# Kernel tuning notes

Measured on AMD Instinct MI355X. Metric: run time of the kernel, lower is better.

The kernel has to match this reference:

```python
import jax, jax.numpy as jnp
import numpy as np

D = 768
H = 12
EPS = 1e-5


def layer_norm(x, g, b):
    mu = jnp.mean(x, axis=-1, keepdims=True)
    var = jnp.var(x, axis=-1, keepdims=True)
    return (x - mu) * jax.lax.rsqrt(var + EPS) * g + b


def setup_inputs() -> dict:
    key = jax.random.key(0)
    ks = jax.random.split(key, 12)
    d, h = D, H
    x = jax.random.normal(ks[0], (4, 1024, d), dtype=jnp.float32)
    # attention projections (per-head dim is full d, per the module)
    s_qkv = (6.0 / (d + d * h)) ** 0.5  # xavier-like scale
    Wq = jax.random.uniform(ks[1], (d, d * h), jnp.float32, -s_qkv, s_qkv)
    Wk = jax.random.uniform(ks[2], (d, d * h), jnp.float32, -s_qkv, s_qkv)
    Wv = jax.random.uniform(ks[3], (d, d * h), jnp.float32, -s_qkv, s_qkv)
    Wu = jax.random.uniform(ks[4], (d * h, d), jnp.float32, -s_qkv, s_qkv)
    bu = jnp.zeros((d,), jnp.float32)
    # MLP
    s1 = (6.0 / (d + 4 * d)) ** 0.5
    W1 = jax.random.uniform(ks[5], (d, 4 * d), jnp.float32, -s1, s1)
    b1 = jax.random.normal(ks[6], (4 * d,), jnp.float32) * 1e-6
    W2 = jax.random.uniform(ks[7], (4 * d, d), jnp.float32, -s1, s1)
    b2 = jax.random.normal(ks[8], (d,), jnp.float32) * 1e-6
    ln1_g = jnp.ones((d,), jnp.float32)
    ln1_b = jnp.zeros((d,), jnp.float32)
    ln2_g = jnp.ones((d,), jnp.float32)
    ln2_b = jnp.zeros((d,), jnp.float32)
    return dict(x=x, Wq=Wq, Wk=Wk, Wv=Wv, Wu=Wu, bu=bu,
                ln1_g=ln1_g, ln1_b=ln1_b, ln2_g=ln2_g, ln2_b=ln2_b,
                W1=W1, b1=b1, W2=W2, b2=b2)


def reference(x, Wq, Wk, Wv, Wu, bu, ln1_g, ln1_b, ln2_g, ln2_b, W1, b1, W2, b2):
    b, n, d = x.shape
    h = H
    # --- pre-LN attention block ---
    res = x
    y = layer_norm(x, ln1_g, ln1_b)
    qs = (y @ Wq).reshape(b, n, h, d)  # per-head dim = d (module quirk)
    ks = (y @ Wk).reshape(b, n, h, d)
    vs = (y @ Wv).reshape(b, n, h, d)
    scores = jnp.einsum('bihd,bjhd->bhij', qs, ks) / (d ** 0.5)
    w = jax.nn.softmax(scores, axis=-1)
    att = jnp.einsum('bhij,bjhd->bihd', w, vs).reshape(b, n, h * d)
    y = att @ Wu + bu
    x = y + res
    # --- pre-LN MLP block (dropout is identity at inference) ---
    res = x
    y = layer_norm(x, ln2_g, ln2_b)
    y = jax.nn.relu(y @ W1 + b1)
    y = y @ W2 + b2
    return y + res
```

## Files before the change

### kernel.cpp

```cpp
#include <hip/hip_runtime.h>
#include <cstdint>
#include <cmath>


typedef __bf16 bf16_t;
typedef __bf16 bf16x8 __attribute__((ext_vector_type(8)));
typedef __bf16 bf16x4 __attribute__((ext_vector_type(4)));
typedef float floatx4 __attribute__((ext_vector_type(4)));

#define DMODEL 768
#define NHEAD  12
#define SEQ    1024
#define NBATCH 4
#define ROWS   (NBATCH*SEQ)
#define DH     (DMODEL*NHEAD)
#define DFF    (4*DMODEL)

template<bool BIAS, bool RES, bool RELU, int OMODE>
__global__ __launch_bounds__(256)
void gemm_v6(const bf16_t* __restrict__ A, const bf16_t* __restrict__ BT,
             void* __restrict__ Cv, int K, int lda, int ldb, int ldc,
             int bdiv, long sa_hi, long sa_lo, long sb_hi, long sb_lo,
             long sc_hi, long sc_lo,
             const float* __restrict__ bias, const float* __restrict__ res,
             int ldres, float alpha)
{
  __shared__ __align__(16) bf16_t As[128*64];
  __shared__ __align__(16) bf16_t Bs[128*64];

  const int tid  = threadIdx.x;
  const int wave = tid >> 6;
  const int lane = tid & 63;
  const int r    = lane & 15;
  const int q    = lane >> 4;

  const int z = blockIdx.z;
  A  += (long)(z / bdiv) * sa_hi + (long)(z % bdiv) * sa_lo;
  BT += (long)(z / bdiv) * sb_hi + (long)(z % bdiv) * sb_lo;
  const long coff = (long)(z / bdiv) * sc_hi + (long)(z % bdiv) * sc_lo;

  const int bm = blockIdx.y * 128;
  const int bn = blockIdx.x * 128;
  const int wm = (wave & 1) * 64;
  const int wn = (wave >> 1) * 64;

  const int blk0 = 2*wave, blk1 = 2*wave + 1;
  const bf16_t* a_src0 = A  + (long)(bm + blk0*16 + r) * lda + q*8;
  const bf16_t* a_src1 = A  + (long)(bm + blk1*16 + r) * lda + q*8;
  const bf16_t* b_src0 = BT + (long)(bn + blk0*16 + r) * ldb + q*8;
  const bf16_t* b_src1 = BT + (long)(bn + blk1*16 + r) * ldb + q*8;
  const int da0 = blk0*512 + lane*8;
  const int da1 = blk1*512 + lane*8;

  const int am = (wave & 1) * 4;
  const int bb = (wave >> 1) * 4;

  floatx4 acc[4][4] = {};

  for (int k0 = 0; k0 < K; k0 += 64) {
    bf16x8 a00 = *(const bf16x8*)(a_src0 + k0);
    bf16x8 a01 = *(const bf16x8*)(a_src0 + k0 + 32);
    bf16x8 a10 = *(const bf16x8*)(a_src1 + k0);
    bf16x8 a11 = *(const bf16x8*)(a_src1 + k0 + 32);
    bf16x8 b00 = *(const bf16x8*)(b_src0 + k0);
    bf16x8 b01 = *(const bf16x8*)(b_src0 + k0 + 32);
    bf16x8 b10 = *(const bf16x8*)(b_src1 + k0);
    bf16x8 b11 = *(const bf16x8*)(b_src1 + k0 + 32);
    *(bf16x8*)(As + da0)        = a00;
    *(bf16x8*)(As + 4096 + da0) = a01;
    *(bf16x8*)(As + da1)        = a10;
    *(bf16x8*)(As + 4096 + da1) = a11;
    *(bf16x8*)(Bs + da0)        = b00;
    *(bf16x8*)(Bs + 4096 + da0) = b01;
    *(bf16x8*)(Bs + da1)        = b10;
    *(bf16x8*)(Bs + 4096 + da1) = b11;
    __syncthreads();
#pragma unroll
    for (int p = 0; p < 2; ++p) {
      bf16x8 afrag[4], bfrag[4];
#pragma unroll
      for (int t = 0; t < 4; ++t) {
        afrag[t] = *(const bf16x8*)(As + p*4096 + (am + t)*512 + lane*8);
        bfrag[t] = *(const bf16x8*)(Bs + p*4096 + (bb + t)*512 + lane*8);
      }
#pragma unroll
      for (int mt = 0; mt < 4; ++mt)
#pragma unroll
        for (int nt = 0; nt < 4; ++nt)
          acc[mt][nt] = __builtin_amdgcn_mfma_f32_16x16x32_bf16(
              afrag[mt], bfrag[nt], acc[mt][nt], 0, 0, 0);
    }
    __syncthreads();
  }

  const int row0 = bm + wm + q*4;
  const int col0 = bn + wn + r;
#pragma unroll
  for (int nt = 0; nt < 4; ++nt) {
    const int col = col0 + nt*16;
    float bv = 0.f;
    if (BIAS) bv = bias[col];
#pragma unroll
    for (int mt = 0; mt < 4; ++mt) {
#pragma unroll
      for (int e = 0; e < 4; ++e) {
        const int rowi = row0 + mt*16 + e;
        float v = acc[mt][nt][e] * alpha;
        if (BIAS) v += bv;
        if (RELU) v = fmaxf(v, 0.f);
        if (RES)  v += res[(long)rowi * ldres + col];
        const long idx = coff + (long)rowi * ldc + col;
        if (OMODE == 0)      ((bf16_t*)Cv)[idx] = (bf16_t)v;
        else if (OMODE == 1) ((float*)Cv)[idx] = v;
        else                 ((float*)Cv)[idx] += v;
      }
    }
  }
}

__global__ void tr_f2b_v6(const float* __restrict__ in, bf16_t* __restrict__ out,
                          int ldi, int ldo)
{
  __shared__ bf16_t tile[32][34];
  const int c0 = blockIdx.x * 32, r0 = blockIdx.y * 32;
  const int tx = threadIdx.x, ty = threadIdx.y;
#pragma unroll
  for (int i = 0; i < 4; ++i)
    tile[ty + 8*i][tx] = (bf16_t)in[(long)(r0 + ty + 8*i) * ldi + c0 + tx];
  __syncthreads();
#pragma unroll
  for (int i = 0; i < 4; ++i)
    out[(long)(c0 + ty + 8*i) * ldo + r0 + tx] = tile[tx][ty + 8*i];
}

__global__ void tr_b_v6(const bf16_t* __restrict__ in, bf16_t* __restrict__ out,
                        int ldi, int ldo, int bdiv,
                        long si_hi, long si_lo, long so_hi, long so_lo)
{
  __shared__ bf16_t tile[32][34];
  const int z = blockIdx.z;
  in  += (long)(z / bdiv) * si_hi + (long)(z % bdiv) * si_lo;
  out += (long)(z / bdiv) * so_hi + (long)(z % bdiv) * so_lo;
  const int c0 = blockIdx.x * 32, r0 = blockIdx.y * 32;
  const int tx = threadIdx.x, ty = threadIdx.y;
#pragma unroll
  for (int i = 0; i < 4; ++i)
    tile[ty + 8*i][tx] = in[(long)(r0 + ty + 8*i) * ldi + c0 + tx];
  __syncthreads();
#pragma unroll
  for (int i = 0; i < 4; ++i)
    out[(long)(c0 + ty + 8*i) * ldo + r0 + tx] = tile[tx][ty + 8*i];
}

__global__ void tr_wh_v6(const float* __restrict__ Wq, const float* __restrict__ Wk,
                         const float* __restrict__ Wv, const float* __restrict__ Wu,
                         bf16_t* __restrict__ WhT, bf16_t* __restrict__ WuTh, int h)
{
  __shared__ bf16_t tile[32][34];
  const int z = blockIdx.z;
  const float* in; bf16_t* out; int ldi;
  if (z < 3) {
    const float* W = (z == 0) ? Wq : (z == 1) ? Wk : Wv;
    in  = W + (long)h * DMODEL;
    ldi = DH;
    out = WhT + (long)z * DMODEL * DMODEL;
  } else {
    in  = Wu + (long)h * DMODEL * DMODEL;
    ldi = DMODEL;
    out = WuTh;
  }
  const int c0 = blockIdx.x * 32, r0 = blockIdx.y * 32;
  const int tx = threadIdx.x, ty = threadIdx.y;
#pragma unroll
  for (int i = 0; i < 4; ++i)
    tile[ty + 8*i][tx] = (bf16_t)in[(long)(r0 + ty + 8*i) * ldi + c0 + tx];
  __syncthreads();
#pragma unroll
  for (int i = 0; i < 4; ++i)
    out[(long)(c0 + ty + 8*i) * DMODEL + r0 + tx] = tile[tx][ty + 8*i];
}

__global__ void cast3_v6(const float* __restrict__ a, const float* __restrict__ b,
                         const float* __restrict__ c,
                         bf16_t* __restrict__ oa, bf16_t* __restrict__ ob,
                         bf16_t* __restrict__ oc)
{
  const float* src = (blockIdx.z == 0) ? a : (blockIdx.z == 1) ? b : c;
  bf16_t* dst      = (blockIdx.z == 0) ? oa : (blockIdx.z == 1) ? ob : oc;
  const long i = ((long)blockIdx.x * 256 + threadIdx.x) * 4;
  float4 v = *(const float4*)(src + i);
  bf16x4 o;
  o[0] = (bf16_t)v.x; o[1] = (bf16_t)v.y; o[2] = (bf16_t)v.z; o[3] = (bf16_t)v.w;
  *(bf16x4*)(dst + i) = o;
}

__global__ void cast1_v6(const float* __restrict__ src, bf16_t* __restrict__ dst)
{
  const long i = ((long)blockIdx.x * 256 + threadIdx.x) * 4;
  float4 v = *(const float4*)(src + i);
  bf16x4 o;
  o[0] = (bf16_t)v.x; o[1] = (bf16_t)v.y; o[2] = (bf16_t)v.z; o[3] = (bf16_t)v.w;
  *(bf16x4*)(dst + i) = o;
}

__global__ void ln_v6(const float* __restrict__ x, const float* __restrict__ g,
                      const float* __restrict__ b, bf16_t* __restrict__ y)
{
  const long row = blockIdx.x;
  const int tid = threadIdx.x;
  const float* xr = x + row * DMODEL;
  float v0 = xr[tid], v1 = xr[tid + 256], v2 = xr[tid + 512];
  float s  = v0 + v1 + v2;
  float ss = v0*v0 + v1*v1 + v2*v2;
  for (int o = 32; o; o >>= 1) { s += __shfl_down(s, o); ss += __shfl_down(ss, o); }
  __shared__ float rs[4], rss[4];
  const int wave = tid >> 6, lane = tid & 63;
  if (lane == 0) { rs[wave] = s; rss[wave] = ss; }
  __syncthreads();
  s  = rs[0] + rs[1] + rs[2] + rs[3];
  ss = rss[0] + rss[1] + rss[2] + rss[3];
  const float inv = 1.0f / (float)DMODEL;
  const float mean = s * inv;
  const float var  = ss * inv - mean * mean;
  const float rstd = rsqrtf(var + 1e-5f);
  bf16_t* yr = y + row * DMODEL;
  yr[tid]       = (bf16_t)(((v0 - mean) * rstd) * g[tid]       + b[tid]);
  yr[tid + 256] = (bf16_t)(((v1 - mean) * rstd) * g[tid + 256] + b[tid + 256]);
  yr[tid + 512] = (bf16_t)(((v2 - mean) * rstd) * g[tid + 512] + b[tid + 512]);
}

__global__ void softmax_v6(bf16_t* __restrict__ S)
{
  const long row = blockIdx.x;
  const int tid = threadIdx.x;
  bf16_t* p = S + row * SEQ + tid * 4;
  bf16x4 v = *(const bf16x4*)p;
  float f0 = (float)v[0], f1 = (float)v[1], f2 = (float)v[2], f3 = (float)v[3];
  float m = fmaxf(fmaxf(f0, f1), fmaxf(f2, f3));
  for (int o = 32; o; o >>= 1) m = fmaxf(m, __shfl_down(m, o));
  __shared__ float rm[4], rsum[4];
  const int wave = tid >> 6, lane = tid & 63;
  if (lane == 0) rm[wave] = m;
  __syncthreads();
  m = fmaxf(fmaxf(rm[0], rm[1]), fmaxf(rm[2], rm[3]));
  float e0 = __expf(f0 - m), e1 = __expf(f1 - m), e2 = __expf(f2 - m), e3 = __expf(f3 - m);
  float s = e0 + e1 + e2 + e3;
  for (int o = 32; o; o >>= 1) s += __shfl_down(s, o);
  if (lane == 0) rsum[wave] = s;
  __syncthreads();
  s = rsum[0] + rsum[1] + rsum[2] + rsum[3];
  const float invs = 1.0f / s;
  bf16x4 o4;
  o4[0] = (bf16_t)(e0 * invs); o4[1] = (bf16_t)(e1 * invs);
  o4[2] = (bf16_t)(e2 * invs); o4[3] = (bf16_t)(e3 * invs);
  *(bf16x4*)p = o4;
}

__global__ void finalize_v6(const float* __restrict__ acc, const float* __restrict__ add,
                            const float* __restrict__ bias, float* __restrict__ o)
{
  const long i = (long)blockIdx.x * 256 + threadIdx.x;
  const int c = (int)(i % DMODEL);
  o[i] = acc[i] + bias[c] + add[i];
}

template<int NP>
__global__ void reduce_v6(const float* __restrict__ p, const float* __restrict__ add,
                          const float* __restrict__ bias, float* __restrict__ o,
                          long plane)
{
  const long i = ((long)blockIdx.x * 256 + threadIdx.x) * 4;
  float4 s = *(const float4*)(p + i);
#pragma unroll
  for (int n = 1; n < NP; ++n) {
    float4 v = *(const float4*)(p + i + (long)n * plane);
    s.x += v.x; s.y += v.y; s.z += v.z; s.w += v.w;
  }
  const int c = (int)(i % DMODEL);
  float4 bv = *(const float4*)(bias + c);
  float4 av = *(const float4*)(add + i);
  float4 r;
  r.x = s.x + bv.x + av.x; r.y = s.y + bv.y + av.y;
  r.z = s.z + bv.z + av.z; r.w = s.w + bv.w + av.w;
  *(float4*)(o + i) = r;
}

extern "C" void kernel_launch(void* const* d_in, const int* in_sizes, int n_in,
                              void* d_out, int out_size, void* d_ws, size_t ws_size,
                              hipStream_t stream)
{
  (void)in_sizes; (void)n_in; (void)out_size;
  const float* x    = (const float*)d_in[0];
  const float* Wq   = (const float*)d_in[1];
  const float* Wk   = (const float*)d_in[2];
  const float* Wv   = (const float*)d_in[3];
  const float* Wu   = (const float*)d_in[4];
  const float* bu   = (const float*)d_in[5];
  const float* ln1g = (const float*)d_in[6];
  const float* ln1b = (const float*)d_in[7];
  const float* ln2g = (const float*)d_in[8];
  const float* ln2b = (const float*)d_in[9];
  const float* W1   = (const float*)d_in[10];
  const float* b1   = (const float*)d_in[11];
  const float* W2   = (const float*)d_in[12];
  const float* b2   = (const float*)d_in[13];
  float* out = (float*)d_out;

  char* ws = (char*)d_ws;
  size_t off = 0;
  auto alloc = [&](size_t bytes) -> void* {
    void* p = (void*)(ws + off);
    off += (bytes + 255) & ~(size_t)255;
    return p;
  };

  const float qk_alpha = 1.0f / sqrtf((float)DMODEL);
  dim3 tb(32, 8);

  const size_t SZ_W   = (size_t)DMODEL * DH * 2;
  const size_t SZ_MT  = (size_t)NHEAD * DMODEL * DMODEL * 2;
  const size_t SZ_Y   = (size_t)ROWS * DMODEL * 2;
  const size_t SZ_X2  = (size_t)ROWS * DMODEL * 4;

  if (ws_size >= (size_t)299e6) {
    bf16_t* MT   = (bf16_t*)alloc(SZ_MT);
    bf16_t* PhT  = (bf16_t*)alloc(SZ_MT);
    bf16_t* y    = (bf16_t*)alloc(SZ_Y);
    float*  x2f  = (float* )alloc(SZ_X2);
    bf16_t* T    = (bf16_t*)alloc((size_t)NBATCH * NHEAD * SEQ * DMODEL * 2);
    bf16_t* S    = (bf16_t*)alloc((size_t)NBATCH * SEQ * NHEAD * SEQ * 2);
    bf16_t* Zt   = (bf16_t*)alloc((size_t)NBATCH * DMODEL * NHEAD * SEQ * 2);
    bf16_t* Wqb  = (bf16_t*)T;
    bf16_t* Wkb  = (bf16_t*)((char*)T + SZ_W);
    bf16_t* Wvb  = (bf16_t*)((char*)T + 2*SZ_W);
    bf16_t* WuT  = (bf16_t*)((char*)T + 3*SZ_W);
    float*  part = (float*)T;
    bf16_t* W1T  = (bf16_t*)S;
    bf16_t* W2T  = (bf16_t*)((char*)S + 4718592);
    bf16_t* t    = (bf16_t*)((char*)S + 9437184);
    float*  partM= (float* )((char*)S + 34603008);
    bf16_t* y2   = (bf16_t*)Zt;

    cast3_v6<<<dim3(6912, 1, 3), 256, 0, stream>>>(Wq, Wk, Wv, Wqb, Wkb, Wvb);
    tr_f2b_v6<<<dim3(DMODEL/32, DH/32), tb, 0, stream>>>(Wu, WuT, DMODEL, DH);
    gemm_v6<false,false,false,0><<<dim3(6, 6, NHEAD), 256, 0, stream>>>(
        Wkb, Wqb, MT, DMODEL, DH, DH, DMODEL, NHEAD,
        0, DMODEL, 0, DMODEL, 0, (long)DMODEL*DMODEL, nullptr, nullptr, 0, 1.0f);
    gemm_v6<false,false,false,0><<<dim3(6, 6, NHEAD), 256, 0, stream>>>(
        WuT, Wvb, PhT, DMODEL, DH, DH, DMODEL, NHEAD,
        0, DMODEL, 0, DMODEL, 0, (long)DMODEL*DMODEL, nullptr, nullptr, 0, 1.0f);

    ln_v6<<<ROWS, 256, 0, stream>>>(x, ln1g, ln1b, y);
    gemm_v6<false,false,false,0><<<dim3(6, 8, NBATCH*NHEAD), 256, 0, stream>>>(
        y, MT, T, DMODEL, DMODEL, DMODEL, DMODEL, NHEAD,
        (long)SEQ*DMODEL, 0, 0, (long)DMODEL*DMODEL,
        (long)NHEAD*SEQ*DMODEL, (long)SEQ*DMODEL, nullptr, nullptr, 0, 1.0f);
    gemm_v6<false,false,false,0><<<dim3(8, 8, NBATCH*NHEAD), 256, 0, stream>>>(
        T, y, S, DMODEL, DMODEL, DMODEL, NHEAD*SEQ, NHEAD,
        (long)NHEAD*SEQ*DMODEL, (long)SEQ*DMODEL, (long)SEQ*DMODEL, 0,
        (long)SEQ*NHEAD*SEQ, (long)SEQ, nullptr, nullptr, 0, qk_alpha);
    softmax_v6<<<NBATCH*SEQ*NHEAD, 256, 0, stream>>>(S);
    gemm_v6<false,false,false,0><<<dim3(8, 6, NBATCH*NHEAD), 256, 0, stream>>>(
        PhT, y, Zt, DMODEL, DMODEL, DMODEL, NHEAD*SEQ, NHEAD,
        0, (long)DMODEL*DMODEL, (long)SEQ*DMODEL, 0,
        (long)DMODEL*NHEAD*SEQ, (long)SEQ, nullptr, nullptr, 0, 1.0f);
    gemm_v6<false,false,false,1><<<dim3(6, 8, 24), 256, 0, stream>>>(
        S, Zt, part, NHEAD*SEQ/6, NHEAD*SEQ, NHEAD*SEQ, DMODEL, NBATCH,
        (long)(NHEAD*SEQ/6), (long)SEQ*NHEAD*SEQ,
        (long)(NHEAD*SEQ/6), (long)DMODEL*NHEAD*SEQ,
        (long)ROWS*DMODEL, (long)SEQ*DMODEL, nullptr, nullptr, 0, 1.0f);
    reduce_v6<6><<<(ROWS*DMODEL)/1024, 256, 0, stream>>>(
        part, x, bu, x2f, (long)ROWS*DMODEL);

    tr_f2b_v6<<<dim3(DFF/32, DMODEL/32), tb, 0, stream>>>(W1, W1T, DFF, DMODEL);
    tr_f2b_v6<<<dim3(DMODEL/32, DFF/32), tb, 0, stream>>>(W2, W2T, DMODEL, DFF);
    ln_v6<<<ROWS, 256, 0, stream>>>(x2f, ln2g, ln2b, y2);
    gemm_v6<true,false,true,0><<<dim3(DFF/128, ROWS/128, 1), 256, 0, stream>>>(
        y2, W1T, t, DMODEL, DMODEL, DMODEL, DFF, 1, 0,0,0,0,0,0, b1, nullptr, 0, 1.0f);
    gemm_v6<false,false,false,1><<<dim3(6, ROWS/128, 2), 256, 0, stream>>>(
        t, W2T, partM, DFF/2, DFF, DFF, DMODEL, 2,
        0, (long)(DFF/2), 0, (long)(DFF/2), 0, (long)ROWS*DMODEL,
        nullptr, nullptr, 0, 1.0f);
    reduce_v6<2><<<(ROWS*DMODEL)/1024, 256, 0, stream>>>(
        partM, x2f, b2, out, (long)ROWS*DMODEL);
  } else if (ws_size >= (size_t)112e6) {
    bf16_t* MT  = (bf16_t*)alloc(SZ_MT);
    bf16_t* PhT = (bf16_t*)alloc(SZ_MT);
    bf16_t* y   = (bf16_t*)alloc(SZ_Y);
    float*  x2f = (float* )alloc(SZ_X2);
    char*   BIG = (char*  )alloc((size_t)62914560);
    bf16_t* T_b  = (bf16_t*)(BIG);
    bf16_t* S_b  = (bf16_t*)(BIG + 18874368);
    bf16_t* Zt_b = (bf16_t*)(BIG + 44040192);
    float*  part = (float* )(BIG);
    bf16_t* Wqb = (bf16_t*)(BIG);
    bf16_t* Wkb = (bf16_t*)(BIG + SZ_W);
    bf16_t* Wvb = (bf16_t*)(BIG + 2*SZ_W);
    bf16_t* WuT = (bf16_t*)(BIG + 3*SZ_W);
    bf16_t* W1T   = (bf16_t*)(BIG);
    bf16_t* W2T   = (bf16_t*)(BIG + 4718592);
    bf16_t* t     = (bf16_t*)(BIG + 9437184);
    float*  partM = (float* )(BIG + 34603008);
    bf16_t* y2    = y;

    cast3_v6<<<dim3(6912, 1, 3), 256, 0, stream>>>(Wq, Wk, Wv, Wqb, Wkb, Wvb);
    tr_f2b_v6<<<dim3(DMODEL/32, DH/32), tb, 0, stream>>>(Wu, WuT, DMODEL, DH);
    gemm_v6<false,false,false,0><<<dim3(6, 6, NHEAD), 256, 0, stream>>>(
        Wkb, Wqb, MT, DMODEL, DH, DH, DMODEL, NHEAD,
        0, DMODEL, 0, DMODEL, 0, (long)DMODEL*DMODEL, nullptr, nullptr, 0, 1.0f);
    gemm_v6<false,false,false,0><<<dim3(6, 6, NHEAD), 256, 0, stream>>>(
        WuT, Wvb, PhT, DMODEL, DH, DH, DMODEL, NHEAD,
        0, DMODEL, 0, DMODEL, 0, (long)DMODEL*DMODEL, nullptr, nullptr, 0, 1.0f);

    ln_v6<<<ROWS, 256, 0, stream>>>(x, ln1g, ln1b, y);
    for (int b = 0; b < NBATCH; ++b) {
      const bf16_t* yb = y + (long)b * SEQ * DMODEL;
      gemm_v6<false,false,false,0><<<dim3(6, 8, NHEAD), 256, 0, stream>>>(
          yb, MT, T_b, DMODEL, DMODEL, DMODEL, DMODEL, NHEAD,
          0, 0, 0, (long)DMODEL*DMODEL, 0, (long)SEQ*DMODEL,
          nullptr, nullptr, 0, 1.0f);
      gemm_v6<false,false,false,0><<<dim3(8, 8, NHEAD), 256, 0, stream>>>(
          T_b, yb, S_b, DMODEL, DMODEL, DMODEL, NHEAD*SEQ, NHEAD,
          0, (long)SEQ*DMODEL, 0, 0, 0, (long)SEQ,
          nullptr, nullptr, 0, qk_alpha);
      softmax_v6<<<NHEAD*SEQ, 256, 0, stream>>>(S_b);
      gemm_v6<false,false,false,0><<<dim3(8, 6, NHEAD), 256, 0, stream>>>(
          PhT, yb, Zt_b, DMODEL, DMODEL, DMODEL, NHEAD*SEQ, NHEAD,
          0, (long)DMODEL*DMODEL, 0, 0, 0, (long)SEQ,
          nullptr, nullptr, 0, 1.0f);
      gemm_v6<false,false,false,1><<<dim3(6, 8, 6), 256, 0, stream>>>(
          S_b, Zt_b, part, NHEAD*SEQ/6, NHEAD*SEQ, NHEAD*SEQ, DMODEL, 6,
          0, (long)(NHEAD*SEQ/6), 0, (long)(NHEAD*SEQ/6), 0, (long)SEQ*DMODEL,
          nullptr, nullptr, 0, 1.0f);
      reduce_v6<6><<<(SEQ*DMODEL)/1024, 256, 0, stream>>>(
          part, x + (long)b*SEQ*DMODEL, bu, x2f + (long)b*SEQ*DMODEL,
          (long)SEQ*DMODEL);
    }

    tr_f2b_v6<<<dim3(DFF/32, DMODEL/32), tb, 0, stream>>>(W1, W1T, DFF, DMODEL);
    tr_f2b_v6<<<dim3(DMODEL/32, DFF/32), tb, 0, stream>>>(W2, W2T, DMODEL, DFF);
    ln_v6<<<ROWS, 256, 0, stream>>>(x2f, ln2g, ln2b, y2);
    gemm_v6<true,false,true,0><<<dim3(DFF/128, ROWS/128, 1), 256, 0, stream>>>(
        y2, W1T, t, DMODEL, DMODEL, DMODEL, DFF, 1, 0,0,0,0,0,0, b1, nullptr, 0, 1.0f);
    gemm_v6<false,false,false,1><<<dim3(6, ROWS/128, 2), 256, 0, stream>>>(
        t, W2T, partM, DFF/2, DFF, DFF, DMODEL, 2,
        0, (long)(DFF/2), 0, (long)(DFF/2), 0, (long)ROWS*DMODEL,
        nullptr, nullptr, 0, 1.0f);
    reduce_v6<2><<<(ROWS*DMODEL)/1024, 256, 0, stream>>>(
        partM, x2f, b2, out, (long)ROWS*DMODEL);
  } else if (ws_size >= (size_t)70e6) {
    bf16_t* MT  = (bf16_t*)alloc(SZ_MT);
    bf16_t* PhT = (bf16_t*)alloc(SZ_MT);
    bf16_t* y   = (bf16_t*)alloc(SZ_Y);
    char*   R   = (char*  )alloc((size_t)33554432);
    bf16_t* WAb = (bf16_t*)(R);
    bf16_t* WBb = (bf16_t*)(R + SZ_W);
    float*  x2f = (float* )(R);
    bf16_t* T_h = (bf16_t*)(R + 12582912);
    bf16_t* S_h = (bf16_t*)(R + 18874368);
    bf16_t* Z_h = (bf16_t*)(R + 27262976);
    bf16_t* W1T = (bf16_t*)(R + 12582912);
    bf16_t* W2T = (bf16_t*)(R + 17301504);
    bf16_t* t   = (bf16_t*)MT;
    bf16_t* y2  = y;

    cast1_v6<<<6912, 256, 0, stream>>>(Wq, WAb);
    cast1_v6<<<6912, 256, 0, stream>>>(Wk, WBb);
    gemm_v6<false,false,false,0><<<dim3(6, 6, NHEAD), 256, 0, stream>>>(
        WBb, WAb, MT, DMODEL, DH, DH, DMODEL, NHEAD,
        0, DMODEL, 0, DMODEL, 0, (long)DMODEL*DMODEL, nullptr, nullptr, 0, 1.0f);
    cast1_v6<<<6912, 256, 0, stream>>>(Wv, WAb);
    tr_f2b_v6<<<dim3(DMODEL/32, DH/32), tb, 0, stream>>>(Wu, WBb, DMODEL, DH);
    gemm_v6<false,false,false,0><<<dim3(6, 6, NHEAD), 256, 0, stream>>>(
        WBb, WAb, PhT, DMODEL, DH, DH, DMODEL, NHEAD,
        0, DMODEL, 0, DMODEL, 0, (long)DMODEL*DMODEL, nullptr, nullptr, 0, 1.0f);

    ln_v6<<<ROWS, 256, 0, stream>>>(x, ln1g, ln1b, y);
    for (int h = 0; h < NHEAD; ++h) {
      const bf16_t* MTh  = MT  + (long)h * DMODEL * DMODEL;
      const bf16_t* PhTh = PhT + (long)h * DMODEL * DMODEL;
      gemm_v6<false,false,false,0><<<dim3(6, ROWS/128, 1), 256, 0, stream>>>(
          y, MTh, T_h, DMODEL, DMODEL, DMODEL, DMODEL, 1,
          0,0,0,0,0,0, nullptr, nullptr, 0, 1.0f);
      gemm_v6<false,false,false,0><<<dim3(8, 8, NBATCH), 256, 0, stream>>>(
          T_h, y, S_h, DMODEL, DMODEL, DMODEL, SEQ, NBATCH,
          0, (long)SEQ*DMODEL, 0, (long)SEQ*DMODEL, 0, (long)SEQ*SEQ,
          nullptr, nullptr, 0, qk_alpha);
      softmax_v6<<<ROWS, 256, 0, stream>>>(S_h);
      gemm_v6<false,false,false,0><<<dim3(8, 6, NBATCH), 256, 0, stream>>>(
          PhTh, y, Z_h, DMODEL, DMODEL, DMODEL, SEQ, NBATCH,
          0, 0, 0, (long)SEQ*DMODEL, 0, (long)DMODEL*SEQ,
          nullptr, nullptr, 0, 1.0f);
      if (h == 0)
        gemm_v6<false,false,false,1><<<dim3(6, 8, NBATCH), 256, 0, stream>>>(
            S_h, Z_h, x2f, SEQ, SEQ, SEQ, DMODEL, NBATCH,
            0, (long)SEQ*SEQ, 0, (long)DMODEL*SEQ, 0, (long)SEQ*DMODEL,
            nullptr, nullptr, 0, 1.0f);
      else
        gemm_v6<false,false,false,2><<<dim3(6, 8, NBATCH), 256, 0, stream>>>(
            S_h, Z_h, x2f, SEQ, SEQ, SEQ, DMODEL, NBATCH,
            0, (long)SEQ*SEQ, 0, (long)DMODEL*SEQ, 0, (long)SEQ*DMODEL,
            nullptr, nullptr, 0, 1.0f);
    }
    finalize_v6<<<(ROWS*DMODEL)/256, 256, 0, stream>>>(x2f, x, bu, x2f);

    tr_f2b_v6<<<dim3(DFF/32, DMODEL/32), tb, 0, stream>>>(W1, W1T, DFF, DMODEL);
    tr_f2b_v6<<<dim3(DMODEL/32, DFF/32), tb, 0, stream>>>(W2, W2T, DMODEL, DFF);
    ln_v6<<<ROWS, 256, 0, stream>>>(x2f, ln2g, ln2b, y2);
    gemm_v6<true,false,true,0><<<dim3(DFF/128, ROWS/128, 1), 256, 0, stream>>>(
        y2, W1T, t, DMODEL, DMODEL, DMODEL, DFF, 1, 0,0,0,0,0,0, b1, nullptr, 0, 1.0f);
    gemm_v6<true,true,false,1><<<dim3(6, ROWS/128, 1), 256, 0, stream>>>(
        t, W2T, out, DFF/2, DFF, DFF, DMODEL, 1, 0,0,0,0,0,0,
        b2, x2f, DMODEL, 1.0f);
    gemm_v6<false,false,false,2><<<dim3(6, ROWS/128, 1), 256, 0, stream>>>(
        t + DFF/2, W2T + DFF/2, out, DFF/2, DFF, DFF, DMODEL, 1, 0,0,0,0,0,0,
        nullptr, nullptr, 0, 1.0f);
  } else {
    bf16_t* W1T   = (bf16_t*)alloc((size_t)DMODEL * DFF * 2);
    bf16_t* W2T   = (bf16_t*)alloc((size_t)DMODEL * DFF * 2);
    bf16_t* y     = (bf16_t*)alloc(SZ_Y);
    float*  x2f   = (float* )alloc(SZ_X2);
    char*   reg1  = (char*)alloc((size_t)3*DMODEL*DMODEL*2 + (size_t)DMODEL*DMODEL*2 + (size_t)SEQ*DMODEL*2);
    bf16_t* WhT   = (bf16_t*)reg1;
    bf16_t* WuTh  = (bf16_t*)(reg1 + (size_t)3*DMODEL*DMODEL*2);
    bf16_t* attb  = (bf16_t*)(reg1 + (size_t)4*DMODEL*DMODEL*2);
    bf16_t* y2    = (bf16_t*)reg1;
    char*   reg2  = (char*)alloc((size_t)SEQ*3*DMODEL*2 + (size_t)DMODEL*SEQ*2 + (size_t)SEQ*SEQ*2);
    bf16_t* QKVb  = (bf16_t*)reg2;
    bf16_t* Vtb   = (bf16_t*)(reg2 + (size_t)SEQ*3*DMODEL*2);
    bf16_t* Sb    = (bf16_t*)(reg2 + (size_t)SEQ*3*DMODEL*2 + (size_t)DMODEL*SEQ*2);
    bf16_t* tslab = (bf16_t*)reg2;

    tr_f2b_v6<<<dim3(DFF/32, DMODEL/32), tb, 0, stream>>>(W1, W1T, DFF, DMODEL);
    tr_f2b_v6<<<dim3(DMODEL/32, DFF/32), tb, 0, stream>>>(W2, W2T, DMODEL, DFF);
    ln_v6<<<ROWS, 256, 0, stream>>>(x, ln1g, ln1b, y);

    const int N3 = 3 * DMODEL;
    for (int h = 0; h < NHEAD; ++h) {
      tr_wh_v6<<<dim3(24, 24, 4), tb, 0, stream>>>(Wq, Wk, Wv, Wu, WhT, WuTh, h);
      for (int b = 0; b < NBATCH; ++b) {
        const bf16_t* yb = y + (size_t)b * SEQ * DMODEL;
        gemm_v6<false,false,false,0><<<dim3(N3/128, SEQ/128, 1), 256, 0, stream>>>(
            yb, WhT, QKVb, DMODEL, DMODEL, DMODEL, N3, 1, 0,0,0,0,0,0,
            nullptr, nullptr, 0, 1.0f);
        tr_b_v6<<<dim3(DMODEL/32, SEQ/32, 1), tb, 0, stream>>>(
            QKVb + 2*DMODEL, Vtb, N3, SEQ, 1, 0,0,0,0);
        gemm_v6<false,false,false,0><<<dim3(SEQ/128, SEQ/128, 1), 256, 0, stream>>>(
            QKVb, QKVb + DMODEL, Sb, DMODEL, N3, N3, SEQ, 1, 0,0,0,0,0,0,
            nullptr, nullptr, 0, qk_alpha);
        softmax_v6<<<SEQ, 256, 0, stream>>>(Sb);
        gemm_v6<false,false,false,0><<<dim3(DMODEL/128, SEQ/128, 1), 256, 0, stream>>>(
            Sb, Vtb, attb, SEQ, SEQ, SEQ, DMODEL, 1, 0,0,0,0,0,0,
            nullptr, nullptr, 0, 1.0f);
        float* x2b = x2f + (size_t)b * SEQ * DMODEL;
        if (h == 0)
          gemm_v6<false,false,false,1><<<dim3(DMODEL/128, SEQ/128, 1), 256, 0, stream>>>(
              attb, WuTh, x2b, DMODEL, DMODEL, DMODEL, DMODEL, 1, 0,0,0,0,0,0,
              nullptr, nullptr, 0, 1.0f);
        else
          gemm_v6<false,false,false,2><<<dim3(DMODEL/128, SEQ/128, 1), 256, 0, stream>>>(
              attb, WuTh, x2b, DMODEL, DMODEL, DMODEL, DMODEL, 1, 0,0,0,0,0,0,
              nullptr, nullptr, 0, 1.0f);
      }
    }
    finalize_v6<<<(ROWS*DMODEL)/256, 256, 0, stream>>>(x2f, x, bu, x2f);
    ln_v6<<<ROWS, 256, 0, stream>>>(x2f, ln2g, ln2b, y2);
    for (int kb = 0; kb < 4; ++kb) {
      gemm_v6<true,false,true,0><<<dim3(DMODEL/128, ROWS/128, 1), 256, 0, stream>>>(
          y2, W1T + (size_t)kb*DMODEL*DMODEL, tslab, DMODEL, DMODEL, DMODEL, DMODEL, 1,
          0,0,0,0,0,0, b1 + kb*DMODEL, nullptr, 0, 1.0f);
      if (kb == 0)
        gemm_v6<true,true,false,1><<<dim3(DMODEL/128, ROWS/128, 1), 256, 0, stream>>>(
            tslab, W2T + (size_t)kb*DMODEL, out, DMODEL, DMODEL, DFF, DMODEL, 1,
            0,0,0,0,0,0, b2, x2f, DMODEL, 1.0f);
      else
        gemm_v6<false,false,false,2><<<dim3(DMODEL/128, ROWS/128, 1), 256, 0, stream>>>(
            tslab, W2T + (size_t)kb*DMODEL, out, DMODEL, DMODEL, DFF, DMODEL, 1,
            0,0,0,0,0,0, nullptr, nullptr, 0, 1.0f);
    }
  }
}
```

Before: 1.170 ms.

## Shrink top-tier workspace by batching T per batch and reducing split-K partials

In the largest-workspace path, the per-head T intermediate is no longer stored for all batches. T is now computed per batch into a reused buffer, and the weight copies are aliased into the S region, which lowers the threshold for that path from 299e6 to 262e6 bytes. The S·Zt split-K drops from 6 to 3 partials, which halves the partial buffer and the reduce traffic but gives fewer blocks. The W2 split-K rises from 2 to 4 partials for more parallelism, at the cost of more partial writes. All kernels are renamed from v6 to v7. Which branch runs depends on the workspace size the harness provides.

Result: faster. 1.047 ms (-10.5%).

```diff
diff --git a/kernel.cpp b/kernel.cpp
--- a/kernel.cpp
+++ b/kernel.cpp
@@ -18,7 +18,7 @@
 
 template<bool BIAS, bool RES, bool RELU, int OMODE>
 __global__ __launch_bounds__(256)
-void gemm_v6(const bf16_t* __restrict__ A, const bf16_t* __restrict__ BT,
+void gemm_v7(const bf16_t* __restrict__ A, const bf16_t* __restrict__ BT,
              void* __restrict__ Cv, int K, int lda, int ldb, int ldc,
              int bdiv, long sa_hi, long sa_lo, long sb_hi, long sb_lo,
              long sc_hi, long sc_lo,
@@ -118,7 +118,7 @@
   }
 }
 
-__global__ void tr_f2b_v6(const float* __restrict__ in, bf16_t* __restrict__ out,
+__global__ void tr_f2b_v7(const float* __restrict__ in, bf16_t* __restrict__ out,
                           int ldi, int ldo)
 {
   __shared__ bf16_t tile[32][34];
@@ -133,7 +133,7 @@
     out[(long)(c0 + ty + 8*i) * ldo + r0 + tx] = tile[tx][ty + 8*i];
 }
 
-__global__ void tr_b_v6(const bf16_t* __restrict__ in, bf16_t* __restrict__ out,
+__global__ void tr_b_v7(const bf16_t* __restrict__ in, bf16_t* __restrict__ out,
                         int ldi, int ldo, int bdiv,
                         long si_hi, long si_lo, long so_hi, long so_lo)
 {
@@ -152,7 +152,7 @@
     out[(long)(c0 + ty + 8*i) * ldo + r0 + tx] = tile[tx][ty + 8*i];
 }
 
-__global__ void tr_wh_v6(const float* __restrict__ Wq, const float* __restrict__ Wk,
+__global__ void tr_wh_v7(const float* __restrict__ Wq, const float* __restrict__ Wk,
                          const float* __restrict__ Wv, const float* __restrict__ Wu,
                          bf16_t* __restrict__ WhT, bf16_t* __restrict__ WuTh, int h)
 {
@@ -180,7 +180,7 @@
     out[(long)(c0 + ty + 8*i) * DMODEL + r0 + tx] = tile[tx][ty + 8*i];
 }
 
-__global__ void cast3_v6(const float* __restrict__ a, const float* __restrict__ b,
+__global__ void cast3_v7(const float* __restrict__ a, const float* __restrict__ b,
                          const float* __restrict__ c,
                          bf16_t* __restrict__ oa, bf16_t* __restrict__ ob,
                          bf16_t* __restrict__ oc)
@@ -194,7 +194,7 @@
   *(bf16x4*)(dst + i) = o;
 }
 
-__global__ void cast1_v6(const float* __restrict__ src, bf16_t* __restrict__ dst)
+__global__ void cast1_v7(const float* __restrict__ src, bf16_t* __restrict__ dst)
 {
   const long i = ((long)blockIdx.x * 256 + threadIdx.x) * 4;
   float4 v = *(const float4*)(src + i);
@@ -203,7 +203,7 @@
   *(bf16x4*)(dst + i) = o;
 }
 
-__global__ void ln_v6(const float* __restrict__ x, const float* __restrict__ g,
+__global__ void ln_v7(const float* __restrict__ x, const float* __restrict__ g,
                       const float* __restrict__ b, bf16_t* __restrict__ y)
 {
   const long row = blockIdx.x;
@@ -229,7 +229,7 @@
   yr[tid + 512] = (bf16_t)(((v2 - mean) * rstd) * g[tid + 512] + b[tid + 512]);
 }
 
-__global__ void softmax_v6(bf16_t* __restrict__ S)
+__global__ void softmax_v7(bf16_t* __restrict__ S)
 {
   const long row = blockIdx.x;
   const int tid = threadIdx.x;
@@ -256,7 +256,7 @@
   *(bf16x4*)p = o4;
 }
 
-__global__ void finalize_v6(const float* __restrict__ acc, const float* __restrict__ add,
+__global__ void finalize_v7(const float* __restrict__ acc, const float* __restrict__ add,
                             const float* __restrict__ bias, float* __restrict__ o)
 {
   const long i = (long)blockIdx.x * 256 + threadIdx.x;
@@ -265,7 +265,7 @@
 }
 
 template<int NP>
-__global__ void reduce_v6(const float* __restrict__ p, const float* __restrict__ add,
+__global__ void reduce_v7(const float* __restrict__ p, const float* __restrict__ add,
                           const float* __restrict__ bias, float* __restrict__ o,
                           long plane)
 {
@@ -322,66 +322,69 @@
   const size_t SZ_Y   = (size_t)ROWS * DMODEL * 2;
   const size_t SZ_X2  = (size_t)ROWS * DMODEL * 4;
 
-  if (ws_size >= (size_t)299e6) {
+  if (ws_size >= (size_t)262e6) {
     bf16_t* MT   = (bf16_t*)alloc(SZ_MT);
     bf16_t* PhT  = (bf16_t*)alloc(SZ_MT);
     bf16_t* y    = (bf16_t*)alloc(SZ_Y);
     float*  x2f  = (float* )alloc(SZ_X2);
-    bf16_t* T    = (bf16_t*)alloc((size_t)NBATCH * NHEAD * SEQ * DMODEL * 2);
+    float*  part = (float* )alloc((size_t)3 * ROWS * DMODEL * 4);
     bf16_t* S    = (bf16_t*)alloc((size_t)NBATCH * SEQ * NHEAD * SEQ * 2);
     bf16_t* Zt   = (bf16_t*)alloc((size_t)NBATCH * DMODEL * NHEAD * SEQ * 2);
-    bf16_t* Wqb  = (bf16_t*)T;
-    bf16_t* Wkb  = (bf16_t*)((char*)T + SZ_W);
-    bf16_t* Wvb  = (bf16_t*)((char*)T + 2*SZ_W);
-    bf16_t* WuT  = (bf16_t*)((char*)T + 3*SZ_W);
-    float*  part = (float*)T;
+    bf16_t* T_b  = (bf16_t*)part;
+    bf16_t* Wqb  = (bf16_t*)S;
+    bf16_t* Wkb  = (bf16_t*)((char*)S + SZ_W);
+    bf16_t* Wvb  = (bf16_t*)((char*)S + 2*SZ_W);
+    bf16_t* WuT  = (bf16_t*)((char*)S + 3*SZ_W);
     bf16_t* W1T  = (bf16_t*)S;
     bf16_t* W2T  = (bf16_t*)((char*)S + 4718592);
     bf16_t* t    = (bf16_t*)((char*)S + 9437184);
     float*  partM= (float* )((char*)S + 34603008);
     bf16_t* y2   = (bf16_t*)Zt;
 
-    cast3_v6<<<dim3(6912, 1, 3), 256, 0, stream>>>(Wq, Wk, Wv, Wqb, Wkb, Wvb);
-    tr_f2b_v6<<<dim3(DMODEL/32, DH/32), tb, 0, stream>>>(Wu, WuT, DMODEL, DH);
-    gemm_v6<false,false,false,0><<<dim3(6, 6, NHEAD), 256, 0, stream>>>(
+    cast3_v7<<<dim3(6912, 1, 3), 256, 0, stream>>>(Wq, Wk, Wv, Wqb, Wkb, Wvb);
+    tr_f2b_v7<<<dim3(DMODEL/32, DH/32), tb, 0, stream>>>(Wu, WuT, DMODEL, DH);
+    gemm_v7<false,false,false,0><<<dim3(6, 6, NHEAD), 256, 0, stream>>>(
         Wkb, Wqb, MT, DMODEL, DH, DH, DMODEL, NHEAD,
         0, DMODEL, 0, DMODEL, 0, (long)DMODEL*DMODEL, nullptr, nullptr, 0, 1.0f);
-    gemm_v6<false,false,false,0><<<dim3(6, 6, NHEAD), 256, 0, stream>>>(
+    gemm_v7<false,false,false,0><<<dim3(6, 6, NHEAD), 256, 0, stream>>>(
         WuT, Wvb, PhT, DMODEL, DH, DH, DMODEL, NHEAD,
         0, DMODEL, 0, DMODEL, 0, (long)DMODEL*DMODEL, nullptr, nullptr, 0, 1.0f);
 
-    ln_v6<<<ROWS, 256, 0, stream>>>(x, ln1g, ln1b, y);
-    gemm_v6<false,false,false,0><<<dim3(6, 8, NBATCH*NHEAD), 256, 0, stream>>>(
-        y, MT, T, DMODEL, DMODEL, DMODEL, DMODEL, NHEAD,
-        (long)SEQ*DMODEL, 0, 0, (long)DMODEL*DMODEL,
-        (long)NHEAD*SEQ*DMODEL, (long)SEQ*DMODEL, nullptr, nullptr, 0, 1.0f);
-    gemm_v6<false,false,false,0><<<dim3(8, 8, NBATCH*NHEAD), 256, 0, stream>>>(
-        T, y, S, DMODEL, DMODEL, DMODEL, NHEAD*SEQ, NHEAD,
-        (long)NHEAD*SEQ*DMODEL, (long)SEQ*DMODEL, (long)SEQ*DMODEL, 0,
-        (long)SEQ*NHEAD*SEQ, (long)SEQ, nullptr, nullptr, 0, qk_alpha);
-    softmax_v6<<<NBATCH*SEQ*NHEAD, 256, 0, stream>>>(S);
-    gemm_v6<false,false,false,0><<<dim3(8, 6, NBATCH*NHEAD), 256, 0, stream>>>(
+    ln_v7<<<ROWS, 256, 0, stream>>>(x, ln1g, ln1b, y);
+    for (int b = 0; b < NBATCH; ++b) {
+      const bf16_t* yb = y + (long)b * SEQ * DMODEL;
+      gemm_v7<false,false,false,0><<<dim3(6, 8, NHEAD), 256, 0, stream>>>(
+          yb, MT, T_b, DMODEL, DMODEL, DMODEL, DMODEL, NHEAD,
+          0, 0, 0, (long)DMODEL*DMODEL, 0, (long)SEQ*DMODEL,
+          nullptr, nullptr, 0, 1.0f);
+      gemm_v7<false,false,false,0><<<dim3(8, 8, NHEAD), 256, 0, stream>>>(
+          T_b, yb, S + (long)b*SEQ*NHEAD*SEQ, DMODEL, DMODEL, DMODEL, NHEAD*SEQ, NHEAD,
+          0, (long)SEQ*DMODEL, 0, 0, 0, (long)SEQ,
+          nullptr, nullptr, 0, qk_alpha);
+    }
+    softmax_v7<<<NBATCH*SEQ*NHEAD, 256, 0, stream>>>(S);
+    gemm_v7<false,false,false,0><<<dim3(8, 6, NBATCH*NHEAD), 256, 0, stream>>>(
         PhT, y, Zt, DMODEL, DMODEL, DMODEL, NHEAD*SEQ, NHEAD,
         0, (long)DMODEL*DMODEL, (long)SEQ*DMODEL, 0,
         (long)DMODEL*NHEAD*SEQ, (long)SEQ, nullptr, nullptr, 0, 1.0f);
-    gemm_v6<false,false,false,1><<<dim3(6, 8, 24), 256, 0, stream>>>(
-        S, Zt, part, NHEAD*SEQ/6, NHEAD*SEQ, NHEAD*SEQ, DMODEL, NBATCH,
-        (long)(NHEAD*SEQ/6), (long)SEQ*NHEAD*SEQ,
-        (long)(NHEAD*SEQ/6), (long)DMODEL*NHEAD*SEQ,
+    gemm_v7<false,false,false,1><<<dim3(6, 8, 12), 256, 0, stream>>>(
+        S, Zt, part, NHEAD*SEQ/3, NHEAD*SEQ, NHEAD*SEQ, DMODEL, NBATCH,
+        (long)(NHEAD*SEQ/3), (long)SEQ*NHEAD*SEQ,
+        (long)(NHEAD*SEQ/3), (long)DMODEL*NHEAD*SEQ,
         (long)ROWS*DMODEL, (long)SEQ*DMODEL, nullptr, nullptr, 0, 1.0f);
-    reduce_v6<6><<<(ROWS*DMODEL)/1024, 256, 0, stream>>>(
+    reduce_v7<3><<<(ROWS*DMODEL)/1024, 256, 0, stream>>>(
         part, x, bu, x2f, (long)ROWS*DMODEL);
 
-    tr_f2b_v6<<<dim3(DFF/32, DMODEL/32), tb, 0, stream>>>(W1, W1T, DFF, DMODEL);
-    tr_f2b_v6<<<dim3(DMODEL/32, DFF/32), tb, 0, stream>>>(W2, W2T, DMODEL, DFF);
-    ln_v6<<<ROWS, 256, 0, stream>>>(x2f, ln2g, ln2b, y2);
-    gemm_v6<true,false,true,0><<<dim3(DFF/128, ROWS/128, 1), 256, 0, stream>>>(
+    tr_f2b_v7<<<dim3(DFF/32, DMODEL/32), tb, 0, stream>>>(W1, W1T, DFF, DMODEL);
+    tr_f2b_v7<<<dim3(DMODEL/32, DFF/32), tb, 0, stream>>>(W2, W2T, DMODEL, DFF);
+    ln_v7<<<ROWS, 256, 0, stream>>>(x2f, ln2g, ln2b, y2);
+    gemm_v7<true,false,true,0><<<dim3(DFF/128, ROWS/128, 1), 256, 0, stream>>>(
         y2, W1T, t, DMODEL, DMODEL, DMODEL, DFF, 1, 0,0,0,0,0,0, b1, nullptr, 0, 1.0f);
-    gemm_v6<false,false,false,1><<<dim3(6, ROWS/128, 2), 256, 0, stream>>>(
-        t, W2T, partM, DFF/2, DFF, DFF, DMODEL, 2,
-        0, (long)(DFF/2), 0, (long)(DFF/2), 0, (long)ROWS*DMODEL,
+    gemm_v7<false,false,false,1><<<dim3(6, ROWS/128, 4), 256, 0, stream>>>(
+        t, W2T, partM, DFF/4, DFF, DFF, DMODEL, 4,
+        0, (long)(DFF/4), 0, (long)(DFF/4), 0, (long)ROWS*DMODEL,
         nullptr, nullptr, 0, 1.0f);
-    reduce_v6<2><<<(ROWS*DMODEL)/1024, 256, 0, stream>>>(
+    reduce_v7<4><<<(ROWS*DMODEL)/1024, 256, 0, stream>>>(
         partM, x2f, b2, out, (long)ROWS*DMODEL);
   } else if (ws_size >= (size_t)112e6) {
     bf16_t* MT  = (bf16_t*)alloc(SZ_MT);
@@ -403,50 +406,50 @@
     float*  partM = (float* )(BIG + 34603008);
     bf16_t* y2    = y;
 
-    cast3_v6<<<dim3(6912, 1, 3), 256, 0, stream>>>(Wq, Wk, Wv, Wqb, Wkb, Wvb);
-    tr_f2b_v6<<<dim3(DMODEL/32, DH/32), tb, 0, stream>>>(Wu, WuT, DMODEL, DH);
-    gemm_v6<false,false,false,0><<<dim3(6, 6, NHEAD), 256, 0, stream>>>(
+    cast3_v7<<<dim3(6912, 1, 3), 256, 0, stream>>>(Wq, Wk, Wv, Wqb, Wkb, Wvb);
+    tr_f2b_v7<<<dim3(DMODEL/32, DH/32), tb, 0, stream>>>(Wu, WuT, DMODEL, DH);
+    gemm_v7<false,false,false,0><<<dim3(6, 6, NHEAD), 256, 0, stream>>>(
         Wkb, Wqb, MT, DMODEL, DH, DH, DMODEL, NHEAD,
         0, DMODEL, 0, DMODEL, 0, (long)DMODEL*DMODEL, nullptr, nullptr, 0, 1.0f);
-    gemm_v6<false,false,false,0><<<dim3(6, 6, NHEAD), 256, 0, stream>>>(
+    gemm_v7<false,false,false,0><<<dim3(6, 6, NHEAD), 256, 0, stream>>>(
         WuT, Wvb, PhT, DMODEL, DH, DH, DMODEL, NHEAD,
         0, DMODEL, 0, DMODEL, 0, (long)DMODEL*DMODEL, nullptr, nullptr, 0, 1.0f);
 
-    ln_v6<<<ROWS, 256, 0, stream>>>(x, ln1g, ln1b, y);
+    ln_v7<<<ROWS, 256, 0, stream>>>(x, ln1g, ln1b, y);
     for (int b = 0; b < NBATCH; ++b) {
       const bf16_t* yb = y + (long)b * SEQ * DMODEL;
-      gemm_v6<false,false,false,0><<<dim3(6, 8, NHEAD), 256, 0, stream>>>(
+      gemm_v7<false,false,false,0><<<dim3(6, 8, NHEAD), 256, 0, stream>>>(
           yb, MT, T_b, DMODEL, DMODEL, DMODEL, DMODEL, NHEAD,
           0, 0, 0, (long)DMODEL*DMODEL, 0, (long)SEQ*DMODEL,
           nullptr, nullptr, 0, 1.0f);
-      gemm_v6<false,false,false,0><<<dim3(8, 8, NHEAD), 256, 0, stream>>>(
+      gemm_v7<false,false,false,0><<<dim3(8, 8, NHEAD), 256, 0, stream>>>(
           T_b, yb, S_b, DMODEL, DMODEL, DMODEL, NHEAD*SEQ, NHEAD,
           0, (long)SEQ*DMODEL, 0, 0, 0, (long)SEQ,
           nullptr, nullptr, 0, qk_alpha);
-      softmax_v6<<<NHEAD*SEQ, 256, 0, stream>>>(S_b);
-      gemm_v6<false,false,false,0><<<dim3(8, 6, NHEAD), 256, 0, stream>>>(
+      softmax_v7<<<NHEAD*SEQ, 256, 0, stream>>>(S_b);
+      gemm_v7<false,false,false,0><<<dim3(8, 6, NHEAD), 256, 0, stream>>>(
           PhT, yb, Zt_b, DMODEL, DMODEL, DMODEL, NHEAD*SEQ, NHEAD,
           0, (long)DMODEL*DMODEL, 0, 0, 0, (long)SEQ,
           nullptr, nullptr, 0, 1.0f);
-      gemm_v6<false,false,false,1><<<dim3(6, 8, 6), 256, 0, stream>>>(
+      gemm_v7<false,false,false,1><<<dim3(6, 8, 6), 256, 0, stream>>>(
           S_b, Zt_b, part, NHEAD*SEQ/6, NHEAD*SEQ, NHEAD*SEQ, DMODEL, 6,
           0, (long)(NHEAD*SEQ/6), 0, (long)(NHEAD*SEQ/6), 0, (long)SEQ*DMODEL,
           nullptr, nullptr, 0, 1.0f);
-      reduce_v6<6><<<(SEQ*DMODEL)/1024, 256, 0, stream>>>(
+      reduce_v7<6><<<(SEQ*DMODEL)/1024, 256, 0, stream>>>(
           part, x + (long)b*SEQ*DMODEL, bu, x2f + (long)b*SEQ*DMODEL,
           (long)SEQ*DMODEL);
     }
 
-    tr_f2b_v6<<<dim3(DFF/32, DMODEL/32), tb, 0, stream>>>(W1, W1T, DFF, DMODEL);
-    tr_f2b_v6<<<dim3(DMODEL/32, DFF/32), tb, 0, stream>>>(W2, W2T, DMODEL, DFF);
-    ln_v6<<<ROWS, 256, 0, stream>>>(x2f, ln2g, ln2b, y2);
-    gemm_v6<true,false,true,0><<<dim3(DFF/128, ROWS/128, 1), 256, 0, stream>>>(
+    tr_f2b_v7<<<dim3(DFF/32, DMODEL/32), tb, 0, stream>>>(W1, W1T, DFF, DMODEL);
+    tr_f2b_v7<<<dim3(DMODEL/32, DFF/32), tb, 0, stream>>>(W2, W2T, DMODEL, DFF);
+    ln_v7<<<ROWS, 256, 0, stream>>>(x2f, ln2g, ln2b, y2);
+    gemm_v7<true,false,true,0><<<dim3(DFF/128, ROWS/128, 1), 256, 0, stream>>>(
         y2, W1T, t, DMODEL, DMODEL, DMODEL, DFF, 1, 0,0,0,0,0,0, b1, nullptr, 0, 1.0f);
-    gemm_v6<false,false,false,1><<<dim3(6, ROWS/128, 2), 256, 0, stream>>>(
+    gemm_v7<false,false,false,1><<<dim3(6, ROWS/128, 2), 256, 0, stream>>>(
         t, W2T, partM, DFF/2, DFF, DFF, DMODEL, 2,
         0, (long)(DFF/2), 0, (long)(DFF/2), 0, (long)ROWS*DMODEL,
         nullptr, nullptr, 0, 1.0f);
-    reduce_v6<2><<<(ROWS*DMODEL)/1024, 256, 0, stream>>>(
+    reduce_v7<2><<<(ROWS*DMODEL)/1024, 256, 0, stream>>>(
         partM, x2f, b2, out, (long)ROWS*DMODEL);
   } else if (ws_size >= (size_t)70e6) {
     bf16_t* MT  = (bf16_t*)alloc(SZ_MT);
@@ -464,55 +467,55 @@
     bf16_t* t   = (bf16_t*)MT;
     bf16_t* y2  = y;
 
-    cast1_v6<<<6912, 256, 0, stream>>>(Wq, WAb);
-    cast1_v6<<<6912, 256, 0, stream>>>(Wk, WBb);
-    gemm_v6<false,false,false,0><<<dim3(6, 6, NHEAD), 256, 0, stream>>>(
+    cast1_v7<<<6912, 256, 0, stream>>>(Wq, WAb);
+    cast1_v7<<<6912, 256, 0, stream>>>(Wk, WBb);
+    gemm_v7<false,false,false,0><<<dim3(6, 6, NHEAD), 256, 0, stream>>>(
         WBb, WAb, MT, DMODEL, DH, DH, DMODEL, NHEAD,
         0, DMODEL, 0, DMODEL, 0, (long)DMODEL*DMODEL, nullptr, nullptr, 0, 1.0f);
-    cast1_v6<<<6912, 256, 0, stream>>>(Wv, WAb);
-    tr_f2b_v6<<<dim3(DMODEL/32, DH/32), tb, 0, stream>>>(Wu, WBb, DMODEL, DH);
-    gemm_v6<false,false,false,0><<<dim3(6, 6, NHEAD), 256, 0, stream>>>(
+    cast1_v7<<<6912, 256, 0, stream>>>(Wv, WAb);
+    tr_f2b_v7<<<dim3(DMODEL/32, DH/32), tb, 0, stream>>>(Wu, WBb, DMODEL, DH);
+    gemm_v7<false,false,false,0><<<dim3(6, 6, NHEAD), 256, 0, stream>>>(
         WBb, WAb, PhT, DMODEL, DH, DH, DMODEL, NHEAD,
         0, DMODEL, 0, DMODEL, 0, (long)DMODEL*DMODEL, nullptr, nullptr, 0, 1.0f);
 
-    ln_v6<<<ROWS, 256, 0, stream>>>(x, ln1g, ln1b, y);
+    ln_v7<<<ROWS, 256, 0, stream>>>(x, ln1g, ln1b, y);
     for (int h = 0; h < NHEAD; ++h) {
       const bf16_t* MTh  = MT  + (long)h * DMODEL * DMODEL;
       const bf16_t* PhTh = PhT + (long)h * DMODEL * DMODEL;
-      gemm_v6<false,false,false,0><<<dim3(6, ROWS/128, 1), 256, 0, stream>>>(
+      gemm_v7<false,false,false,0><<<dim3(6, ROWS/128, 1), 256, 0, stream>>>(
           y, MTh, T_h, DMODEL, DMODEL, DMODEL, DMODEL, 1,
           0,0,0,0,0,0, nullptr, nullptr, 0, 1.0f);
-      gemm_v6<false,false,false,0><<<dim3(8, 8, NBATCH), 256, 0, stream>>>(
+      gemm_v7<false,false,false,0><<<dim3(8, 8, NBATCH), 256, 0, stream>>>(
           T_h, y, S_h, DMODEL, DMODEL, DMODEL, SEQ, NBATCH,
           0, (long)SEQ*DMODEL, 0, (long)SEQ*DMODEL, 0, (long)SEQ*SEQ,
           nullptr, nullptr, 0, qk_alpha);
-      softmax_v6<<<ROWS, 256, 0, stream>>>(S_h);
-      gemm_v6<false,false,false,0><<<dim3(8, 6, NBATCH), 256, 0, stream>>>(
+      softmax_v7<<<ROWS, 256, 0, stream>>>(S_h);
+      gemm_v7<false,false,false,0><<<dim3(8, 6, NBATCH), 256, 0, stream>>>(
           PhTh, y, Z_h, DMODEL, DMODEL, DMODEL, SEQ, NBATCH,
           0, 0, 0, (long)SEQ*DMODEL, 0, (long)DMODEL*SEQ,
           nullptr, nullptr, 0, 1.0f);
       if (h == 0)
-        gemm_v6<false,false,false,1><<<dim3(6, 8, NBATCH), 256, 0, stream>>>(
+        gemm_v7<false,false,false,1><<<dim3(6, 8, NBATCH), 256, 0, stream>>>(
             S_h, Z_h, x2f, SEQ, SEQ, SEQ, DMODEL, NBATCH,
             0, (long)SEQ*SEQ, 0, (long)DMODEL*SEQ, 0, (long)SEQ*DMODEL,
             nullptr, nullptr, 0, 1.0f);
       else
-        gemm_v6<false,false,false,2><<<dim3(6, 8, NBATCH), 256, 0, stream>>>(
+        gemm_v7<false,false,false,2><<<dim3(6, 8, NBATCH), 256, 0, stream>>>(
             S_h, Z_h, x2f, SEQ, SEQ, SEQ, DMODEL, NBATCH,
             0, (long)SEQ*SEQ, 0, (long)DMODEL*SEQ, 0, (long)SEQ*DMODEL,
             nullptr, nullptr, 0, 1.0f);
     }
-    finalize_v6<<<(ROWS*DMODEL)/256, 256, 0, stream>>>(x2f, x, bu, x2f);
-
-    tr_f2b_v6<<<dim3(DFF/32, DMODEL/32), tb, 0, stream>>>(W1, W1T, DFF, DMODEL);
-    tr_f2b_v6<<<dim3(DMODEL/32, DFF/32), tb, 0, stream>>>(W2, W2T, DMODEL, DFF);
-    ln_v6<<<ROWS, 256, 0, stream>>>(x2f, ln2g, ln2b, y2);
-    gemm_v6<true,false,true,0><<<dim3(DFF/128, ROWS/128, 1), 256, 0, stream>>>(
+    finalize_v7<<<(ROWS*DMODEL)/256, 256, 0, stream>>>(x2f, x, bu, x2f);
+
+    tr_f2b_v7<<<dim3(DFF/32, DMODEL/32), tb, 0, stream>>>(W1, W1T, DFF, DMODEL);
+    tr_f2b_v7<<<dim3(DMODEL/32, DFF/32), tb, 0, stream>>>(W2, W2T, DMODEL, DFF);
+    ln_v7<<<ROWS, 256, 0, stream>>>(x2f, ln2g, ln2b, y2);
+    gemm_v7<true,false,true,0><<<dim3(DFF/128, ROWS/128, 1), 256, 0, stream>>>(
         y2, W1T, t, DMODEL, DMODEL, DMODEL, DFF, 1, 0,0,0,0,0,0, b1, nullptr, 0, 1.0f);
-    gemm_v6<true,true,false,1><<<dim3(6, ROWS/128, 1), 256, 0, stream>>>(
+    gemm_v7<true,true,false,1><<<dim3(6, ROWS/128, 1), 256, 0, stream>>>(
         t, W2T, out, DFF/2, DFF, DFF, DMODEL, 1, 0,0,0,0,0,0,
         b2, x2f, DMODEL, 1.0f);
-    gemm_v6<false,false,false,2><<<dim3(6, ROWS/128, 1), 256, 0, stream>>>(
+    gemm_v7<false,false,false,2><<<dim3(6, ROWS/128, 1), 256, 0, stream>>>(
         t + DFF/2, W2T + DFF/2, out, DFF/2, DFF, DFF, DMODEL, 1, 0,0,0,0,0,0,
         nullptr, nullptr, 0, 1.0f);
   } else {
@@ -531,50 +534,50 @@
     bf16_t* Sb    = (bf16_t*)(reg2 + (size_t)SEQ*3*DMODEL*2 + (size_t)DMODEL*SEQ*2);
     bf16_t* tslab = (bf16_t*)reg2;
 
-    tr_f2b_v6<<<dim3(DFF/32, DMODEL/32), tb, 0, stream>>>(W1, W1T, DFF, DMODEL);
-    tr_f2b_v6<<<dim3(DMODEL/32, DFF/32), tb, 0, stream>>>(W2, W2T, DMODEL, DFF);
-    ln_v6<<<ROWS, 256, 0, stream>>>(x, ln1g, ln1b, y);
+    tr_f2b_v7<<<dim3(DFF/32, DMODEL/32), tb, 0, stream>>>(W1, W1T, DFF, DMODEL);
+    tr_f2b_v7<<<dim3(DMODEL/32, DFF/32), tb, 0, stream>>>(W2, W2T, DMODEL, DFF);
+    ln_v7<<<ROWS, 256, 0, stream>>>(x, ln1g, ln1b, y);
 
     const int N3 = 3 * DMODEL;
     for (int h = 0; h < NHEAD; ++h) {
-      tr_wh_v6<<<dim3(24, 24, 4), tb, 0, stream>>>(Wq, Wk, Wv, Wu, WhT, WuTh, h);
+      tr_wh_v7<<<dim3(24, 24, 4), tb, 0, stream>>>(Wq, Wk, Wv, Wu, WhT, WuTh, h);
       for (int b = 0; b < NBATCH; ++b) {
         const bf16_t* yb = y + (size_t)b * SEQ * DMODEL;
-        gemm_v6<false,false,false,0><<<dim3(N3/128, SEQ/128, 1), 256, 0, stream>>>(
+        gemm_v7<false,false,false,0><<<dim3(N3/128, SEQ/128, 1), 256, 0, stream>>>(
             yb, WhT, QKVb, DMODEL, DMODEL, DMODEL, N3, 1, 0,0,0,0,0,0,
             nullptr, nullptr, 0, 1.0f);
-        tr_b_v6<<<dim3(DMODEL/32, SEQ/32, 1), tb, 0, stream>>>(
+        tr_b_v7<<<dim3(DMODEL/32, SEQ/32, 1), tb, 0, stream>>>(
             QKVb + 2*DMODEL, Vtb, N3, SEQ, 1, 0,0,0,0);
-        gemm_v6<false,false,false,0><<<dim3(SEQ/128, SEQ/128, 1), 256, 0, stream>>>(
+        gemm_v7<false,false,false,0><<<dim3(SEQ/128, SEQ/128, 1), 256, 0, stream>>>(
             QKVb, QKVb + DMODEL, Sb, DMODEL, N3, N3, SEQ, 1, 0,0,0,0,0,0,
             nullptr, nullptr, 0, qk_alpha);
-        softmax_v6<<<SEQ, 256, 0, stream>>>(Sb);
-        gemm_v6<false,false,false,0><<<dim3(DMODEL/128, SEQ/128, 1), 256, 0, stream>>>(
+        softmax_v7<<<SEQ, 256, 0, stream>>>(Sb);
+        gemm_v7<false,false,false,0><<<dim3(DMODEL/128, SEQ/128, 1), 256, 0, stream>>>(
             Sb, Vtb, attb, SEQ, SEQ, SEQ, DMODEL, 1, 0,0,0,0,0,0,
             nullptr, nullptr, 0, 1.0f);
         float* x2b = x2f + (size_t)b * SEQ * DMODEL;
         if (h == 0)
-          gemm_v6<false,false,false,1><<<dim3(DMODEL/128, SEQ/128, 1), 256, 0, stream>>>(
+          gemm_v7<false,false,false,1><<<dim3(DMODEL/128, SEQ/128, 1), 256, 0, stream>>>(
               attb, WuTh, x2b, DMODEL, DMODEL, DMODEL, DMODEL, 1, 0,0,0,0,0,0,
               nullptr, nullptr, 0, 1.0f);
         else
-          gemm_v6<false,false,false,2><<<dim3(DMODEL/128, SEQ/128, 1), 256, 0, stream>>>(
+          gemm_v7<false,false,false,2><<<dim3(DMODEL/128, SEQ/128, 1), 256, 0, stream>>>(
               attb, WuTh, x2b, DMODEL, DMODEL, DMODEL, DMODEL, 1, 0,0,0,0,0,0,
               nullptr, nullptr, 0, 1.0f);
       }
     }
-    finalize_v6<<<(ROWS*DMODEL)/256, 256, 0, stream>>>(x2f, x, bu, x2f);
-    ln_v6<<<ROWS, 256, 0, stream>>>(x2f, ln2g, ln2b, y2);
+    finalize_v7<<<(ROWS*DMODEL)/256, 256, 0, stream>>>(x2f, x, bu, x2f);
+    ln_v7<<<ROWS, 256, 0, stream>>>(x2f, ln2g, ln2b, y2);
     for (int kb = 0; kb < 4; ++kb) {
-      gemm_v6<true,false,true,0><<<dim3(DMODEL/128, ROWS/128, 1), 256, 0, stream>>>(
+      gemm_v7<true,false,true,0><<<dim3(DMODEL/128, ROWS/128, 1), 256, 0, stream>>>(
           y2, W1T + (size_t)kb*DMODEL*DMODEL, tslab, DMODEL, DMODEL, DMODEL, DMODEL, 1,
           0,0,0,0,0,0, b1 + kb*DMODEL, nullptr, 0, 1.0f);
       if (kb == 0)
-        gemm_v6<true,true,false,1><<<dim3(DMODEL/128, ROWS/128, 1), 256, 0, stream>>>(
+        gemm_v7<true,true,false,1><<<dim3(DMODEL/128, ROWS/128, 1), 256, 0, stream>>>(
             tslab, W2T + (size_t)kb*DMODEL, out, DMODEL, DMODEL, DFF, DMODEL, 1,
             0,0,0,0,0,0, b2, x2f, DMODEL, 1.0f);
       else
-        gemm_v6<false,false,false,2><<<dim3(DMODEL/128, ROWS/128, 1), 256, 0, stream>>>(
+        gemm_v7<false,false,false,2><<<dim3(DMODEL/128, ROWS/128, 1), 256, 0, stream>>>(
             tslab, W2T + (size_t)kb*DMODEL, out, DMODEL, DMODEL, DFF, DMODEL, 1,
             0,0,0,0,0,0, nullptr, nullptr, 0, 1.0f);
     }
```
